# Kernel optimization log

Measured on AMD Instinct MI355X. Metric: run time of the kernel, lower is better.

The kernel has to match this reference:

```python
import jax, jax.numpy as jnp
import numpy as np


def setup_inputs() -> dict:
    key = jax.random.key(0)
    k1, k2 = jax.random.split(key)
    features = jax.random.normal(k1, (2048, 2, 4096), dtype=jnp.float32)
    labels = jax.random.randint(k2, (2048,), 0, 8)  # int labels 0..7
    return {"features": features, "labels": labels}


def reference(features, labels):
    # contrast_mode='one': anchors are view 0 only
    anchor = features[:, 0]                     # [N, d]
    N, d = anchor.shape
    logp = jax.nn.log_softmax(anchor, axis=1)    # [N, d]
    p = jnp.exp(logp)                            # softmax probs

    # Pairwise symmetric KL via one matmul.
    # F.kl_div(log p, q, reduction='batchmean') on 1-D vectors of length d
    # = sum_k q_k (log q_k - log p_k) / d, so
    # sym_kl(i,j) = (C[i,i] + C[j,j] - C[i,j] - C[j,i]) / (2d)
    # where C[i,j] = sum_k p_i[k] * logp_j[k].
    C = p @ logp.T                               # [N, N]
    diag = jnp.diagonal(C)                       # sum p log p per row
    M = (diag[:, None] + diag[None, :] - C - C.T) / (2.0 * d)

    triu = jnp.triu(jnp.ones((N, N), dtype=bool), k=1)  # unordered pairs i<j
    same = labels[:, None] == labels[None, :]
    same_sum = jnp.sum(jnp.where(triu & same, M, 0.0))
    diff_sum = jnp.sum(jnp.where(triu & ~same, M, 0.0))
    return same_sum / diff_sum
```

## Files before the change

kernel.cpp:

```cpp
#include <hip/hip_runtime.h>
#include <cmath>

#define N_ROWS 2048
#define DIM 4096
#define ROW_STRIDE 8192
#define NCLS 8
#define NY   32
#define SLICE_WORDS (2*NCLS*DIM)

__device__ __forceinline__ float wred_sum(float v){
  #pragma unroll
  for(int o=32;o>0;o>>=1) v += __shfl_xor(v,o,64);
  return v;
}
__device__ __forceinline__ float wred_max(float v){
  #pragma unroll
  for(int o=32;o>0;o>>=1) v = fmaxf(v,__shfl_xor(v,o,64));
  return v;
}

__global__ __launch_bounds__(256) void k1_rowstats(
    const float* __restrict__ feat, float* __restrict__ lse,
    float* __restrict__ diag){
  const int t = threadIdx.x;
  const int row = blockIdx.x;
  const int wave = t>>6, lane = t&63;
  const float4* x4 = (const float4*)(feat + (size_t)row * ROW_STRIDE);
  float4 v[4];
  #pragma unroll
  for(int k=0;k<4;k++) v[k] = x4[t + k*256];

  __shared__ float red[8];
  float m = -INFINITY;
  #pragma unroll
  for(int k=0;k<4;k++)
    m = fmaxf(m, fmaxf(fmaxf(v[k].x,v[k].y), fmaxf(v[k].z,v[k].w)));
  m = wred_max(m);
  if(lane==0) red[wave] = m;
  __syncthreads();
  m = fmaxf(fmaxf(red[0],red[1]), fmaxf(red[2],red[3]));
  __syncthreads();
  float s = 0.f, t1 = 0.f;
  #pragma unroll
  for(int k=0;k<4;k++){
    float a=v[k].x-m, b=v[k].y-m, c=v[k].z-m, d2=v[k].w-m;
    float ea=__expf(a), eb=__expf(b), ec=__expf(c), ed=__expf(d2);
    s  += ea + eb + ec + ed;
    t1 += a*ea + b*eb + c*ec + d2*ed;
  }
  s  = wred_sum(s);
  t1 = wred_sum(t1);
  if(lane==0){ red[wave] = s; red[4+wave] = t1; }
  __syncthreads();
  if(t==0){
    float S  = red[0]+red[1]+red[2]+red[3];
    float T1 = red[4]+red[5]+red[6]+red[7];
    float lg = __logf(S);
    lse[row]  = m + lg;
    diag[row] = T1/S - lg;
  }
}

__global__ __launch_bounds__(256,2) void k2_accum(
    const float* __restrict__ feat, const float* __restrict__ lse,
    const int* __restrict__ labels,
    float* __restrict__ PLslices){
  const int d = blockIdx.x * 256 + threadIdx.x;
  const int y = blockIdx.y;
  const int r0 = y * 64;
  float P0=0,P1=0,P2=0,P3=0,P4=0,P5=0,P6=0,P7=0;
  float L0=0,L1=0,L2=0,L3=0,L4=0,L5=0,L6=0,L7=0;
  const float* col = feat + (size_t)r0 * ROW_STRIDE + d;
  for(int ib=0; ib<4; ib++){
    float xs[16];
    #pragma unroll
    for(int j=0;j<16;j++)
      xs[j] = col[(size_t)(ib*16+j) * ROW_STRIDE];
    #pragma unroll
    for(int j=0;j<16;j++){
      const int r = r0 + ib*16 + j;
      float v = xs[j] - lse[r];
      float e = __expf(v);
      int lab = __builtin_amdgcn_readfirstlane(labels[r]);
      switch(lab){
        case 0: P0+=e; L0+=v; break;
        case 1: P1+=e; L1+=v; break;
        case 2: P2+=e; L2+=v; break;
        case 3: P3+=e; L3+=v; break;
        case 4: P4+=e; L4+=v; break;
        case 5: P5+=e; L5+=v; break;
        case 6: P6+=e; L6+=v; break;
        default: P7+=e; L7+=v; break;
      }
    }
  }
  float* slice = PLslices + (size_t)y * SLICE_WORDS;
  float* Ps = slice;
  float* Ls = slice + NCLS*DIM;
  Ps[0*DIM+d]=P0; Ls[0*DIM+d]=L0;
  Ps[1*DIM+d]=P1; Ls[1*DIM+d]=L1;
  Ps[2*DIM+d]=P2; Ls[2*DIM+d]=L2;
  Ps[3*DIM+d]=P3; Ls[3*DIM+d]=L3;
  Ps[4*DIM+d]=P4; Ls[4*DIM+d]=L4;
  Ps[5*DIM+d]=P5; Ls[5*DIM+d]=L5;
  Ps[6*DIM+d]=P6; Ls[6*DIM+d]=L6;
  Ps[7*DIM+d]=P7; Ls[7*DIM+d]=L7;
}

__global__ __launch_bounds__(256) void k2b_reduce(
    const float* __restrict__ PLslices, float* __restrict__ PLfinal){
  const int gid = blockIdx.x * 256 + threadIdx.x;
  float s = 0.f;
  #pragma unroll 8
  for(int y=0;y<NY;y++)
    s += PLslices[(size_t)y * SLICE_WORDS + gid];
  PLfinal[gid] = s;
}

__global__ __launch_bounds__(1024) void k3_final(
    const float* __restrict__ diag, const int* __restrict__ labels,
    const float* __restrict__ Pbuf, const float* __restrict__ Lbuf,
    float* __restrict__ out){
  const int t = threadIdx.x;
  const int wave = t>>6, lane = t&63;

  __shared__ double sD[16][8];
  __shared__ int    sN[16][8];
  __shared__ double sS[16], sA[16];

  double Dl[8]; int Nl[8];
  #pragma unroll
  for(int c=0;c<8;c++){ Dl[c]=0.0; Nl[c]=0; }
  for(int i=t;i<N_ROWS;i+=1024){
    int lab = labels[i];
    double dg = (double)diag[i];
    #pragma unroll
    for(int c=0;c<8;c++){
      if(lab==c){ Dl[c]+=dg; Nl[c]++; }
    }
  }
  #pragma unroll
  for(int c=0;c<8;c++){
    #pragma unroll
    for(int o=32;o>0;o>>=1){
      Dl[c] += __shfl_xor(Dl[c],o,64);
      Nl[c] += __shfl_xor(Nl[c],o,64);
    }
  }
  if(lane==0){
    #pragma unroll
    for(int c=0;c<8;c++){ sD[wave][c]=Dl[c]; sN[wave][c]=Nl[c]; }
  }

  double acc_same=0.0, acc_all=0.0;
  {
    const int base = t*4;
    double ps0=0,ps1=0,ps2=0,ps3=0, ls0=0,ls1=0,ls2=0,ls3=0;
    #pragma unroll
    for(int c=0;c<8;c++){
      float4 p4 = *(const float4*)&Pbuf[c*DIM + base];
      float4 l4 = *(const float4*)&Lbuf[c*DIM + base];
      acc_same += (double)p4.x*(double)l4.x + (double)p4.y*(double)l4.y
                + (double)p4.z*(double)l4.z + (double)p4.w*(double)l4.w;
      ps0 += p4.x; ps1 += p4.y; ps2 += p4.z; ps3 += p4.w;
      ls0 += l4.x; ls1 += l4.y; ls2 += l4.z; ls3 += l4.w;
    }
    acc_all = ps0*ls0 + ps1*ls1 + ps2*ls2 + ps3*ls3;
  }
  #pragma unroll
  for(int o=32;o>0;o>>=1){
    acc_same += __shfl_xor(acc_same,o,64);
    acc_all  += __shfl_xor(acc_all,o,64);
  }
  if(lane==0){ sS[wave]=acc_same; sA[wave]=acc_all; }
  __syncthreads();

  if(t==0){
    double D[8]; int Ncnt[8];
    #pragma unroll
    for(int c=0;c<8;c++){
      double d0=0.0; int n0=0;
      #pragma unroll
      for(int w=0;w<16;w++){ d0 += sD[w][c]; n0 += sN[w][c]; }
      D[c]=d0; Ncnt[c]=n0;
    }
    double S_same=0.0, S_all=0.0;
    #pragma unroll
    for(int w=0;w<16;w++){ S_same += sS[w]; S_all += sA[w]; }
    double same_num=0.0, diff_num=0.0;
    #pragma unroll
    for(int c=0;c<8;c++){
      same_num += (double)Ncnt[c]*D[c];
      diff_num += (double)(N_ROWS - Ncnt[c])*D[c];
    }
    same_num -= S_same;
    diff_num -= (S_all - S_same);
    out[0] = (float)(same_num/diff_num);
  }
}

extern "C" void kernel_launch(void* const* d_in, const int* in_sizes, int n_in,
                              void* d_out, int out_size, void* d_ws, size_t ws_size,
                              hipStream_t stream){
  const float* feat   = (const float*)d_in[0];
  const int*   labels = (const int*)d_in[1];
  float* out = (float*)d_out;
  float* ws  = (float*)d_ws;
  float* lse     = ws;
  float* diag    = ws + N_ROWS;
  float* PLfinal = ws + 2*N_ROWS;
  float* PLslices= PLfinal + SLICE_WORDS;

  k1_rowstats<<<N_ROWS, 256, 0, stream>>>(feat, lse, diag);
  k2_accum<<<dim3(DIM/256, NY), 256, 0, stream>>>(feat, lse, labels, PLslices);
  k2b_reduce<<<SLICE_WORDS/256, 256, 0, stream>>>(PLslices, PLfinal);
  k3_final<<<1, 1024, 0, stream>>>(diag, labels, PLfinal, PLfinal + NCLS*DIM, out);
}
```

Baseline: 118.1 us.

## Fuse all stages into one cooperative kernel with grid-wide syncs

```diff
diff --git a/kernel.cpp b/kernel.cpp
--- a/kernel.cpp
+++ b/kernel.cpp
@@ -1,5 +1,8 @@
 #include <hip/hip_runtime.h>
+#include <hip/hip_cooperative_groups.h>
 #include <cmath>
+
+namespace cg = cooperative_groups;
 
 #define N_ROWS 2048
 #define DIM 4096
@@ -7,6 +10,13 @@
 #define NCLS 8
 #define NY   32
 #define SLICE_WORDS (2*NCLS*DIM)
+#define NBLK 512
+
+#define OFF_LSE    0
+#define OFF_DIAG   (N_ROWS)
+#define OFF_PL     (2*N_ROWS)
+#define OFF_SLICES (OFF_PL + SLICE_WORDS)
+#define OFF_SCAL   (OFF_SLICES + NY*SLICE_WORDS)
 
 __device__ __forceinline__ float wred_sum(float v){
   #pragma unroll
@@ -17,6 +27,191 @@
   #pragma unroll
   for(int o=32;o>0;o>>=1) v = fmaxf(v,__shfl_xor(v,o,64));
   return v;
+}
+__device__ __forceinline__ double wred_sum_d(double v){
+  #pragma unroll
+  for(int o=32;o>0;o>>=1) v += __shfl_xor(v,o,64);
+  return v;
+}
+
+__global__ __launch_bounds__(256,2) void mega(
+    const float* __restrict__ feat, const int* __restrict__ labels,
+    float* __restrict__ ws, float* __restrict__ out){
+  cg::grid_group grid = cg::this_grid();
+  const int b = blockIdx.x, t = threadIdx.x;
+  const int wave = t>>6, lane = t&63;
+
+  float* lse    = ws + OFF_LSE;
+  float* diag   = ws + OFF_DIAG;
+  float* PL     = ws + OFF_PL;
+  float* slices = ws + OFF_SLICES;
+  double* Dsum  = (double*)(ws + OFF_SCAL);
+  double* Spart = Dsum + 8;
+  double* Apart = Spart + 16;
+  int*    Ncnt  = (int*)(Apart + 16);
+
+  __shared__ float  redf[8];
+  __shared__ double sD[4][8];
+  __shared__ int    sN[4][8];
+  __shared__ double sS[4], sA[4];
+
+  for(int rr=0; rr<4; rr++){
+    const int row = b*4 + rr;
+    const float4* x4 = (const float4*)(feat + (size_t)row * ROW_STRIDE);
+    float4 v[4];
+    #pragma unroll
+    for(int k=0;k<4;k++) v[k] = x4[t + k*256];
+    float m = -INFINITY;
+    #pragma unroll
+    for(int k=0;k<4;k++)
+      m = fmaxf(m, fmaxf(fmaxf(v[k].x,v[k].y), fmaxf(v[k].z,v[k].w)));
+    m = wred_max(m);
+    if(lane==0) redf[wave] = m;
+    __syncthreads();
+    m = fmaxf(fmaxf(redf[0],redf[1]), fmaxf(redf[2],redf[3]));
+    __syncthreads();
+    float s = 0.f, t1 = 0.f;
+    #pragma unroll
+    for(int k=0;k<4;k++){
+      float a=v[k].x-m, b2=v[k].y-m, c=v[k].z-m, d2=v[k].w-m;
+      float ea=__expf(a), eb=__expf(b2), ec=__expf(c), ed=__expf(d2);
+      s  += ea + eb + ec + ed;
+      t1 += a*ea + b2*eb + c*ec + d2*ed;
+    }
+    s  = wred_sum(s);
+    t1 = wred_sum(t1);
+    if(lane==0){ redf[wave] = s; redf[4+wave] = t1; }
+    __syncthreads();
+    if(t==0){
+      float S  = redf[0]+redf[1]+redf[2]+redf[3];
+      float T1 = redf[4]+redf[5]+redf[6]+redf[7];
+      float lg = __logf(S);
+      lse[row]  = m + lg;
+      diag[row] = T1/S - lg;
+    }
+    __syncthreads();
+  }
+  grid.sync();
+
+  {
+    const int x = b & 15, y = b >> 4;
+    const int d = x * 256 + t;
+    const int r0 = y * 64;
+    float P0=0,P1=0,P2=0,P3=0,P4=0,P5=0,P6=0,P7=0;
+    float L0=0,L1=0,L2=0,L3=0,L4=0,L5=0,L6=0,L7=0;
+    const float* col = feat + (size_t)r0 * ROW_STRIDE + d;
+    for(int ib=0; ib<4; ib++){
+      float xs[16];
+      #pragma unroll
+      for(int j=0;j<16;j++)
+        xs[j] = col[(size_t)(ib*16+j) * ROW_STRIDE];
+      #pragma unroll
+      for(int j=0;j<16;j++){
+        const int r = r0 + ib*16 + j;
+        float vv = xs[j] - lse[r];
+        float e = __expf(vv);
+        int lab = __builtin_amdgcn_readfirstlane(labels[r]);
+        switch(lab){
+          case 0: P0+=e; L0+=vv; break;
+          case 1: P1+=e; L1+=vv; break;
+          case 2: P2+=e; L2+=vv; break;
+          case 3: P3+=e; L3+=vv; break;
+          case 4: P4+=e; L4+=vv; break;
+          case 5: P5+=e; L5+=vv; break;
+          case 6: P6+=e; L6+=vv; break;
+          default: P7+=e; L7+=vv; break;
+        }
+      }
+    }
+    float* slice = slices + (size_t)y * SLICE_WORDS;
+    float* Ps = slice;
+    float* Ls = slice + NCLS*DIM;
+    Ps[0*DIM+d]=P0; Ls[0*DIM+d]=L0;
+    Ps[1*DIM+d]=P1; Ls[1*DIM+d]=L1;
+    Ps[2*DIM+d]=P2; Ls[2*DIM+d]=L2;
+    Ps[3*DIM+d]=P3; Ls[3*DIM+d]=L3;
+    Ps[4*DIM+d]=P4; Ls[4*DIM+d]=L4;
+    Ps[5*DIM+d]=P5; Ls[5*DIM+d]=L5;
+    Ps[6*DIM+d]=P6; Ls[6*DIM+d]=L6;
+    Ps[7*DIM+d]=P7; Ls[7*DIM+d]=L7;
+  }
+  grid.sync();
+
+  if(b < 256){
+    const int gid = b*256 + t;
+    float s = 0.f;
+    #pragma unroll 8
+    for(int y=0;y<NY;y++)
+      s += slices[(size_t)y * SLICE_WORDS + gid];
+    PL[gid] = s;
+  } else if(b == 256){
+    double Dl[8]; int Nl[8];
+    #pragma unroll
+    for(int c=0;c<8;c++){ Dl[c]=0.0; Nl[c]=0; }
+    for(int i=t;i<N_ROWS;i+=256){
+      int lab = labels[i];
+      double dg = (double)diag[i];
+      #pragma unroll
+      for(int c=0;c<8;c++){
+        if(lab==c){ Dl[c]+=dg; Nl[c]++; }
+      }
+    }
+    #pragma unroll
+    for(int c=0;c<8;c++){
+      #pragma unroll
+      for(int o=32;o>0;o>>=1){
+        Dl[c] += __shfl_xor(Dl[c],o,64);
+        Nl[c] += __shfl_xor(Nl[c],o,64);
+      }
+    }
+    if(lane==0){
+      #pragma unroll
+      for(int c=0;c<8;c++){ sD[wave][c]=Dl[c]; sN[wave][c]=Nl[c]; }
+    }
+    __syncthreads();
+    if(t<8){
+      Dsum[t] = sD[0][t]+sD[1][t]+sD[2][t]+sD[3][t];
+      Ncnt[t] = sN[0][t]+sN[1][t]+sN[2][t]+sN[3][t];
+    }
+  }
+  grid.sync();
+
+  if(b < 16){
+    const int d = b*256 + t;
+    double acc_same=0.0, ps=0.0, ls=0.0;
+    #pragma unroll
+    for(int c=0;c<8;c++){
+      float p  = PL[c*DIM + d];
+      float lq = PL[NCLS*DIM + c*DIM + d];
+      acc_same += (double)p*(double)lq;
+      ps += (double)p; ls += (double)lq;
+    }
+    double acc_all = ps*ls;
+    acc_same = wred_sum_d(acc_same);
+    acc_all  = wred_sum_d(acc_all);
+    if(lane==0){ sS[wave]=acc_same; sA[wave]=acc_all; }
+    __syncthreads();
+    if(t==0){
+      Spart[b] = sS[0]+sS[1]+sS[2]+sS[3];
+      Apart[b] = sA[0]+sA[1]+sA[2]+sA[3];
+    }
+  }
+  grid.sync();
+
+  if(b==0 && t==0){
+    double S_same=0.0, S_all=0.0;
+    #pragma unroll
+    for(int i=0;i<16;i++){ S_same += Spart[i]; S_all += Apart[i]; }
+    double same_num=0.0, diff_num=0.0;
+    #pragma unroll
+    for(int c=0;c<8;c++){
+      same_num += (double)Ncnt[c]*Dsum[c];
+      diff_num += (double)(N_ROWS - Ncnt[c])*Dsum[c];
+    }
+    same_num -= S_same;
+    diff_num -= (S_all - S_same);
+    out[0] = (float)(same_num/diff_num);
+  }
 }
 
 __global__ __launch_bounds__(256) void k1_rowstats(
@@ -29,7 +224,6 @@
   float4 v[4];
   #pragma unroll
   for(int k=0;k<4;k++) v[k] = x4[t + k*256];
-
   __shared__ float red[8];
   float m = -INFINITY;
   #pragma unroll
@@ -123,11 +317,9 @@
     float* __restrict__ out){
   const int t = threadIdx.x;
   const int wave = t>>6, lane = t&63;
-
   __shared__ double sD[16][8];
   __shared__ int    sN[16][8];
   __shared__ double sS[16], sA[16];
-
   double Dl[8]; int Nl[8];
   #pragma unroll
   for(int c=0;c<8;c++){ Dl[c]=0.0; Nl[c]=0; }
@@ -151,7 +343,6 @@
     #pragma unroll
     for(int c=0;c<8;c++){ sD[wave][c]=Dl[c]; sN[wave][c]=Nl[c]; }
   }
-
   double acc_same=0.0, acc_all=0.0;
   {
     const int base = t*4;
@@ -174,15 +365,14 @@
   }
   if(lane==0){ sS[wave]=acc_same; sA[wave]=acc_all; }
   __syncthreads();
-
   if(t==0){
-    double D[8]; int Ncnt[8];
+    double D[8]; int Ncnt2[8];
     #pragma unroll
     for(int c=0;c<8;c++){
       double d0=0.0; int n0=0;
       #pragma unroll
       for(int w=0;w<16;w++){ d0 += sD[w][c]; n0 += sN[w][c]; }
-      D[c]=d0; Ncnt[c]=n0;
+      D[c]=d0; Ncnt2[c]=n0;
     }
     double S_same=0.0, S_all=0.0;
     #pragma unroll
@@ -190,8 +380,8 @@
     double same_num=0.0, diff_num=0.0;
     #pragma unroll
     for(int c=0;c<8;c++){
-      same_num += (double)Ncnt[c]*D[c];
-      diff_num += (double)(N_ROWS - Ncnt[c])*D[c];
+      same_num += (double)Ncnt2[c]*D[c];
+      diff_num += (double)(N_ROWS - Ncnt2[c])*D[c];
     }
     same_num -= S_same;
     diff_num -= (S_all - S_same);
@@ -206,13 +396,19 @@
   const int*   labels = (const int*)d_in[1];
   float* out = (float*)d_out;
   float* ws  = (float*)d_ws;
-  float* lse     = ws;
-  float* diag    = ws + N_ROWS;
-  float* PLfinal = ws + 2*N_ROWS;
-  float* PLslices= PLfinal + SLICE_WORDS;
-
-  k1_rowstats<<<N_ROWS, 256, 0, stream>>>(feat, lse, diag);
-  k2_accum<<<dim3(DIM/256, NY), 256, 0, stream>>>(feat, lse, labels, PLslices);
-  k2b_reduce<<<SLICE_WORDS/256, 256, 0, stream>>>(PLslices, PLfinal);
-  k3_final<<<1, 1024, 0, stream>>>(diag, labels, PLfinal, PLfinal + NCLS*DIM, out);
-}
+
+  void* args[] = { (void*)&feat, (void*)&labels, (void*)&ws, (void*)&out };
+  hipError_t err = hipLaunchCooperativeKernel(
+      (const void*)mega, dim3(NBLK), dim3(256), args, 0, stream);
+
+  if(err != hipSuccess){
+    float* lse      = ws + OFF_LSE;
+    float* diag     = ws + OFF_DIAG;
+    float* PLfinal  = ws + OFF_PL;
+    float* PLslices = ws + OFF_SLICES;
+    k1_rowstats<<<N_ROWS, 256, 0, stream>>>(feat, lse, diag);
+    k2_accum<<<dim3(DIM/256, NY), 256, 0, stream>>>(feat, lse, labels, PLslices);
+    k2b_reduce<<<SLICE_WORDS/256, 256, 0, stream>>>(PLslices, PLfinal);
+    k3_final<<<1, 1024, 0, stream>>>(diag, labels, PLfinal, PLfinal + NCLS*DIM, out);
+  }
+}
```

Measured after the change: 353.6 us. 2.99x slower.

## Fuse slice reduction and final dot into one kernel with last-block finish

Applied to the files above, without the earlier changes.

```diff
diff --git a/kernel.cpp b/kernel.cpp
--- a/kernel.cpp
+++ b/kernel.cpp
@@ -7,6 +7,12 @@
 #define NCLS 8
 #define NY   32
 #define SLICE_WORDS (2*NCLS*DIM)
+#define K2C_BLOCKS 128
+
+#define OFF_LSE    0
+#define OFF_DIAG   (N_ROWS)
+#define OFF_SLICES (2*N_ROWS)
+#define OFF_SCAL   (OFF_SLICES + NY*SLICE_WORDS)
 
 __device__ __forceinline__ float wred_sum(float v){
   #pragma unroll
@@ -21,10 +27,14 @@
 
 __global__ __launch_bounds__(256) void k1_rowstats(
     const float* __restrict__ feat, float* __restrict__ lse,
-    float* __restrict__ diag){
+    float* __restrict__ diag, double* __restrict__ scal){
   const int t = threadIdx.x;
   const int row = blockIdx.x;
   const int wave = t>>6, lane = t&63;
+  if(row==0 && t==0){
+    scal[0]=0.0; scal[1]=0.0;
+    ((unsigned int*)(scal+2))[0] = 0u;
+  }
   const float4* x4 = (const float4*)(feat + (size_t)row * ROW_STRIDE);
   float4 v[4];
   #pragma unroll
@@ -107,91 +117,92 @@
   Ps[7*DIM+d]=P7; Ls[7*DIM+d]=L7;
 }
 
-__global__ __launch_bounds__(256) void k2b_reduce(
-    const float* __restrict__ PLslices, float* __restrict__ PLfinal){
-  const int gid = blockIdx.x * 256 + threadIdx.x;
-  float s = 0.f;
+__global__ __launch_bounds__(256) void k2c_dot(
+    const float* __restrict__ PLslices,
+    const float* __restrict__ diag, const int* __restrict__ labels,
+    double* __restrict__ scal, float* __restrict__ out){
+  const int b = blockIdx.x, t = threadIdx.x;
+  const int wave = t>>6, lane = t&63;
+  const int c = t>>5;
+  const int j = t&31;
+  const int d = b*32 + j;
+  unsigned int* count = (unsigned int*)(scal+2);
+
+  float Pf=0.f, Lf=0.f;
+  const float* basep = PLslices + c*DIM + d;
+  const float* basel = basep + NCLS*DIM;
   #pragma unroll 8
-  for(int y=0;y<NY;y++)
-    s += PLslices[(size_t)y * SLICE_WORDS + gid];
-  PLfinal[gid] = s;
-}
-
-__global__ __launch_bounds__(1024) void k3_final(
-    const float* __restrict__ diag, const int* __restrict__ labels,
-    const float* __restrict__ Pbuf, const float* __restrict__ Lbuf,
-    float* __restrict__ out){
-  const int t = threadIdx.x;
-  const int wave = t>>6, lane = t&63;
-
-  __shared__ double sD[16][8];
-  __shared__ int    sN[16][8];
-  __shared__ double sS[16], sA[16];
-
+  for(int y=0;y<NY;y++){
+    Pf += basep[(size_t)y*SLICE_WORDS];
+    Lf += basel[(size_t)y*SLICE_WORDS];
+  }
+  double acc_same = (double)Pf * (double)Lf;
+
+  __shared__ float sPf[8][32], sLf[8][32];
+  __shared__ double sS[4];
+  sPf[c][j]=Pf; sLf[c][j]=Lf;
+  __syncthreads();
+  double acc_all = 0.0;
+  if(t < 32){
+    double ps=0.0, ls=0.0;
+    #pragma unroll
+    for(int cc=0;cc<8;cc++){ ps += (double)sPf[cc][t]; ls += (double)sLf[cc][t]; }
+    acc_all = ps*ls;
+  }
+  #pragma unroll
+  for(int o=32;o>0;o>>=1) acc_same += __shfl_xor(acc_same,o,64);
+  if(lane==0) sS[wave]=acc_same;
+  #pragma unroll
+  for(int o=16;o>0;o>>=1) acc_all += __shfl_xor(acc_all,o,64);
+  __syncthreads();
+  if(t==0){
+    atomicAdd(&scal[0], sS[0]+sS[1]+sS[2]+sS[3]);
+    atomicAdd(&scal[1], acc_all);
+    __threadfence();
+  }
+  __syncthreads();
+
+  __shared__ unsigned int is_last;
+  if(t==0) is_last = (atomicAdd(count, 1u) == K2C_BLOCKS-1) ? 1u : 0u;
+  __syncthreads();
+  if(!is_last) return;
+
+  __shared__ double sD[4][8];
+  __shared__ int    sN[4][8];
   double Dl[8]; int Nl[8];
   #pragma unroll
-  for(int c=0;c<8;c++){ Dl[c]=0.0; Nl[c]=0; }
-  for(int i=t;i<N_ROWS;i+=1024){
+  for(int cc=0;cc<8;cc++){ Dl[cc]=0.0; Nl[cc]=0; }
+  for(int i=t;i<N_ROWS;i+=256){
     int lab = labels[i];
     double dg = (double)diag[i];
     #pragma unroll
-    for(int c=0;c<8;c++){
-      if(lab==c){ Dl[c]+=dg; Nl[c]++; }
-    }
-  }
-  #pragma unroll
-  for(int c=0;c<8;c++){
+    for(int cc=0;cc<8;cc++){
+      if(lab==cc){ Dl[cc]+=dg; Nl[cc]++; }
+    }
+  }
+  #pragma unroll
+  for(int cc=0;cc<8;cc++){
     #pragma unroll
     for(int o=32;o>0;o>>=1){
-      Dl[c] += __shfl_xor(Dl[c],o,64);
-      Nl[c] += __shfl_xor(Nl[c],o,64);
+      Dl[cc] += __shfl_xor(Dl[cc],o,64);
+      Nl[cc] += __shfl_xor(Nl[cc],o,64);
     }
   }
   if(lane==0){
     #pragma unroll
-    for(int c=0;c<8;c++){ sD[wave][c]=Dl[c]; sN[wave][c]=Nl[c]; }
-  }
-
-  double acc_same=0.0, acc_all=0.0;
-  {
-    const int base = t*4;
-    double ps0=0,ps1=0,ps2=0,ps3=0, ls0=0,ls1=0,ls2=0,ls3=0;
-    #pragma unroll
-    for(int c=0;c<8;c++){
-      float4 p4 = *(const float4*)&Pbuf[c*DIM + base];
-      float4 l4 = *(const float4*)&Lbuf[c*DIM + base];
-      acc_same += (double)p4.x*(double)l4.x + (double)p4.y*(double)l4.y
-                + (double)p4.z*(double)l4.z + (double)p4.w*(double)l4.w;
-      ps0 += p4.x; ps1 += p4.y; ps2 += p4.z; ps3 += p4.w;
-      ls0 += l4.x; ls1 += l4.y; ls2 += l4.z; ls3 += l4.w;
-    }
-    acc_all = ps0*ls0 + ps1*ls1 + ps2*ls2 + ps3*ls3;
-  }
-  #pragma unroll
-  for(int o=32;o>0;o>>=1){
-    acc_same += __shfl_xor(acc_same,o,64);
-    acc_all  += __shfl_xor(acc_all,o,64);
-  }
-  if(lane==0){ sS[wave]=acc_same; sA[wave]=acc_all; }
-  __syncthreads();
-
+    for(int cc=0;cc<8;cc++){ sD[wave][cc]=Dl[cc]; sN[wave][cc]=Nl[cc]; }
+  }
+  __syncthreads();
   if(t==0){
-    double D[8]; int Ncnt[8];
-    #pragma unroll
-    for(int c=0;c<8;c++){
-      double d0=0.0; int n0=0;
-      #pragma unroll
-      for(int w=0;w<16;w++){ d0 += sD[w][c]; n0 += sN[w][c]; }
-      D[c]=d0; Ncnt[c]=n0;
-    }
-    double S_same=0.0, S_all=0.0;
-    #pragma unroll
-    for(int w=0;w<16;w++){ S_same += sS[w]; S_all += sA[w]; }
+    double S_same = atomicAdd(&scal[0], 0.0);
+    double S_all  = atomicAdd(&scal[1], 0.0);
     double same_num=0.0, diff_num=0.0;
     #pragma unroll
-    for(int c=0;c<8;c++){
-      same_num += (double)Ncnt[c]*D[c];
-      diff_num += (double)(N_ROWS - Ncnt[c])*D[c];
+    for(int cc=0;cc<8;cc++){
+      double Dc = sD[0][cc]+sD[1][cc]+sD[2][cc]+sD[3][cc];
+      int    nc = sN[0][cc]+sN[1][cc]+sN[2][cc]+sN[3][cc];
+      same_num += (double)nc*Dc;
+      diff_num += (double)(N_ROWS - nc)*Dc;
     }
     same_num -= S_same;
     diff_num -= (S_all - S_same);
@@ -206,13 +217,12 @@
   const int*   labels = (const int*)d_in[1];
   float* out = (float*)d_out;
   float* ws  = (float*)d_ws;
-  float* lse     = ws;
-  float* diag    = ws + N_ROWS;
-  float* PLfinal = ws + 2*N_ROWS;
-  float* PLslices= PLfinal + SLICE_WORDS;
-
-  k1_rowstats<<<N_ROWS, 256, 0, stream>>>(feat, lse, diag);
+  float*  lse      = ws + OFF_LSE;
+  float*  diag     = ws + OFF_DIAG;
+  float*  PLslices = ws + OFF_SLICES;
+  double* scal     = (double*)(ws + OFF_SCAL);
+
+  k1_rowstats<<<N_ROWS, 256, 0, stream>>>(feat, lse, diag, scal);
   k2_accum<<<dim3(DIM/256, NY), 256, 0, stream>>>(feat, lse, labels, PLslices);
-  k2b_reduce<<<SLICE_WORDS/256, 256, 0, stream>>>(PLslices, PLfinal);
-  k3_final<<<1, 1024, 0, stream>>>(diag, labels, PLfinal, PLfinal + NCLS*DIM, out);
-}
+  k2c_dot<<<K2C_BLOCKS, 256, 0, stream>>>(PLslices, diag, labels, scal, out);
+}
```

Result: no change. 119.1 us (+0.9%).
